# Kernel tuning notes

Measured on AMD Instinct MI355X. Metric: run time of the kernel, lower is better.

## Reference

```python
import jax, jax.numpy as jnp
import numpy as np

D_MODEL = 1024
D_INNER = 4096
K = 127
B, L = 2, 4096

def setup_inputs() -> dict:
    key = jax.random.key(0)
    k1, k2, k3, k4, k5 = jax.random.split(key, 5)
    x = jax.random.normal(k1, (B, L, D_MODEL), dtype=jnp.float32)
    # in_proj: Linear(d, 2*m) -> weight [2m, d] (torch convention)
    w_in = jax.random.normal(k2, (2 * D_INNER, D_MODEL), dtype=jnp.float32) * (1.0 / np.sqrt(D_MODEL))
    # depthwise conv weight: [m, 1, k] in torch; store as [m, k]
    w_dw = jax.random.normal(k3, (D_INNER, K), dtype=jnp.float32) * (1.0 / np.sqrt(K))
    b_dw = jax.random.normal(k4, (D_INNER,), dtype=jnp.float32) * 0.01
    # out_proj: Linear(m, d) -> weight [d, m]
    w_out = jax.random.normal(k5, (D_MODEL, D_INNER), dtype=jnp.float32) * (1.0 / np.sqrt(D_INNER))
    return {"x": x, "w_in": w_in, "w_dw": w_dw, "b_dw": b_dw, "w_out": w_out}

def _causal_dwconv(v, w_dw, b_dw):
    # v: [B, L, m]; causal depthwise conv with kernel K
    # pad K-1 on the left only (equivalent to torch pad=K-1 then [..., :L])
    v_bcl = jnp.transpose(v, (0, 2, 1))  # [B, m, L]
    out = jax.lax.conv_general_dilated(
        v_bcl,
        w_dw[:, None, :],  # [m, 1, K]
        window_strides=(1,),
        padding=[(K - 1, 0)],
        feature_group_count=D_INNER,
        dimension_numbers=("NCH", "OIH", "NCH"),
    )
    out = out + b_dw[None, :, None]
    return jnp.transpose(out, (0, 2, 1))  # [B, L, m]

def reference(x, w_in, w_dw, b_dw, w_out):
    vg = jnp.einsum("bld,ed->ble", x, w_in)  # [B, L, 2m]
    v, g = jnp.split(vg, 2, axis=-1)
    v = _causal_dwconv(v, w_dw, b_dw)
    y = jax.nn.silu(v) * jax.nn.silu(g)
    return jnp.einsum("blm,dm->bld", y, w_out)
```

## Files before the change

### kernel.cpp

```cpp
#include <hip/hip_runtime.h>
#include <hip/hip_bf16.h>
#include <cstdint>
#include <cstddef>

typedef __fp16 f16_t;
typedef __attribute__((ext_vector_type(8))) __fp16 f16x8;
typedef __attribute__((ext_vector_type(4))) __fp16 f16x4;
typedef __attribute__((ext_vector_type(2))) __fp16 h2_t;
typedef __attribute__((ext_vector_type(4))) float floatx4;

__device__ __forceinline__ void async_copy_16B(const void* g, void* l) {
  __builtin_amdgcn_global_load_lds(
      (const __attribute__((address_space(1))) void*)g,
      (__attribute__((address_space(3))) void*)l, 16, 0, 0);
}

__global__ __launch_bounds__(256) void prep(
    const float* __restrict__ x, const float* __restrict__ w_in,
    const float* __restrict__ w_out, const float* __restrict__ w_dw,
    f16_t* __restrict__ x_h, f16_t* __restrict__ wi_h,
    f16_t* __restrict__ wo_h, h2_t* __restrict__ wp) {
  const int tid = blockIdx.x * 256 + threadIdx.x;
  if (tid < 5242880) {
    const float* src;
    f16_t* dst;
    int off;
    if (tid < 2097152) {
      src = x; dst = x_h; off = tid;
    } else if (tid < 4194304) {
      src = w_in; dst = wi_h; off = tid - 2097152;
    } else {
      src = w_out; dst = wo_h; off = tid - 4194304;
    }
    const float4 v = *(const float4*)(src + (size_t)off * 4);
    f16x4 o;
    o.x = (f16_t)v.x; o.y = (f16_t)v.y; o.z = (f16_t)v.z; o.w = (f16_t)v.w;
    *(f16x4*)(dst + (size_t)off * 4) = o;
  } else {
    const int idx = tid - 5242880;
    if (idx < 128 * 4096) {
      const int p = idx >> 12;
      const int c = idx & 4095;
      float a, b;
      if (p < 126) {
        a = w_dw[c * 127 + p]; b = w_dw[c * 127 + p + 1];
      } else if (p == 126) {
        a = w_dw[c * 127 + 126]; b = 0.f;
      } else {
        a = 0.f; b = w_dw[c * 127 + 0];
      }
      h2_t w;
      w.x = (f16_t)a; w.y = (f16_t)b;
      wp[idx] = w;
    }
  }
}

template <int BN_, typename OutT>
__global__ __launch_bounds__(256) void gemm_bt64(
    const f16_t* __restrict__ A, const f16_t* __restrict__ B,
    OutT* __restrict__ C, int M, int N, int K) {
  constexpr int BM_ = 128;
  constexpr int FI = (BN_ == 128) ? 4 : 2;
  constexpr int FJ = 4;
  constexpr int ACH = BM_ * 8;
  constexpr int CH = (BM_ + BN_) * 8;
  constexpr int CPT = CH / 256;

  __shared__ f16_t smem[(BM_ + BN_) * 64];
  f16_t* const As0 = smem;
  f16_t* const As1 = smem + BM_ * 32;
  f16_t* const Bs0 = smem + BM_ * 64;
  f16_t* const Bs1 = smem + BM_ * 64 + BN_ * 32;

  const int t = threadIdx.x;
  const int lane = t & 63;
  const int wave = t >> 6;
  const int m0 = blockIdx.y * BM_;
  const int n0 = blockIdx.x * BN_;
  const int wr = (BN_ == 128) ? (wave >> 1) * 64 : wave * 32;
  const int wc = (BN_ == 128) ? (wave & 1) * 64 : 0;
  const int fr = lane & 15;
  const int fk = (lane >> 4) * 8;

  floatx4 acc[FI][FJ] = {};

  const int kTiles = K / 64;
  for (int kt = 0; kt < kTiles; ++kt) {
    const int k0 = kt * 64;
    __syncthreads();
#pragma unroll
    for (int it = 0; it < CPT; ++it) {
      const int p = it * 256 + t;
      const f16_t* gsrc;
      if (p < BM_ * 4) {
        const int row = p >> 2, kc = (p & 3) * 8;
        gsrc = A + (size_t)(m0 + row) * K + k0 + kc;
      } else if (p < ACH) {
        const int q = p - BM_ * 4;
        const int row = q >> 2, kc = 32 + (q & 3) * 8;
        gsrc = A + (size_t)(m0 + row) * K + k0 + kc;
      } else if (p < ACH + BN_ * 4) {
        const int q = p - ACH;
        const int row = q >> 2, kc = (q & 3) * 8;
        gsrc = B + (size_t)(n0 + row) * K + k0 + kc;
      } else {
        const int q = p - ACH - BN_ * 4;
        const int row = q >> 2, kc = 32 + (q & 3) * 8;
        gsrc = B + (size_t)(n0 + row) * K + k0 + kc;
      }
      async_copy_16B(gsrc, smem + p * 8);
    }
    __syncthreads();

    f16x8 af[FI][2], bfr[FJ][2];
#pragma unroll
    for (int i = 0; i < FI; ++i) {
      const int r = (wr + i * 16 + fr) * 32 + fk;
      af[i][0] = *(const f16x8*)(As0 + r);
      af[i][1] = *(const f16x8*)(As1 + r);
    }
#pragma unroll
    for (int j = 0; j < FJ; ++j) {
      const int r = (wc + j * 16 + fr) * 32 + fk;
      bfr[j][0] = *(const f16x8*)(Bs0 + r);
      bfr[j][1] = *(const f16x8*)(Bs1 + r);
    }
#pragma unroll
    for (int h = 0; h < 2; ++h)
#pragma unroll
      for (int i = 0; i < FI; ++i)
#pragma unroll
        for (int j = 0; j < FJ; ++j)
          acc[i][j] = __builtin_amdgcn_mfma_f32_16x16x32_f16(
              af[i][h], bfr[j][h], acc[i][j], 0, 0, 0);
  }

  const int cr = (lane >> 4) * 4;
  const int cc = lane & 15;
#pragma unroll
  for (int i = 0; i < FI; ++i)
#pragma unroll
    for (int j = 0; j < FJ; ++j)
#pragma unroll
      for (int r = 0; r < 4; ++r) {
        const int row = m0 + wr + i * 16 + cr + r;
        const int col = n0 + wc + j * 16 + cc;
        C[(size_t)row * N + col] = (OutT)acc[i][j][r];
      }
}

#define CONV_L 128
#define CPAIRS 127

__global__ __launch_bounds__(256) void conv_gate(
    const f16_t* __restrict__ vg, const h2_t* __restrict__ wp,
    const float* __restrict__ b_dw, f16_t* __restrict__ y) {
  __shared__ uint32_t vtp[CPAIRS * 64];
  __shared__ uint32_t wpl[128 * 64];
  const int t = threadIdx.x;
  const int lane = t & 63;
  const int wave = t >> 6;
  const int c0 = blockIdx.x * 64;
  const int lt = blockIdx.y & 31;
  const int b = blockIdx.y >> 5;
  const int l0 = lt * CONV_L;

#pragma unroll
  for (int it = 0; it < 8; ++it) {
    const int q = it * 256 + t;
    async_copy_16B(wp + (size_t)(q >> 4) * 4096 + c0 + (q & 15) * 4,
                   wpl + q * 4);
  }
  for (int q = t; q < CPAIRS * 8; q += 256) {
    const int m = q >> 3;
    const int oc = (q & 7) * 8;
    const int le = l0 - 126 + 2 * m;
    uint4 a = make_uint4(0u, 0u, 0u, 0u);
    uint4 bb = make_uint4(0u, 0u, 0u, 0u);
    if (le >= 0) {
      const size_t base = (size_t)(b * 4096 + le) * 8192 + c0 + oc;
      a = *(const uint4*)(vg + base);
      bb = *(const uint4*)(vg + base + 8192);
    }
    uint32_t* dst = vtp + m * 64 + oc;
    const uint32_t aw[4] = {a.x, a.y, a.z, a.w};
    const uint32_t bw[4] = {bb.x, bb.y, bb.z, bb.w};
#pragma unroll
    for (int i = 0; i < 4; ++i) {
      dst[2 * i] = (aw[i] & 0xFFFFu) | (bw[i] << 16);
      dst[2 * i + 1] = (aw[i] >> 16) | (bw[i] & 0xFFFF0000u);
    }
  }
  __syncthreads();

  const int c = c0 + lane;
  const float bias = b_dw[c];
  float acc[32];
#pragma unroll
  for (int i = 0; i < 32; ++i) acc[i] = bias;

  const uint32_t* vbase = vtp + wave * 16 * 64 + lane;
  const uint32_t* wbase = wpl + lane;

  h2_t ring[17];
#pragma unroll
  for (int m = 0; m < 17; ++m)
    ring[m] = __builtin_bit_cast(h2_t, vbase[m * 64]);

  {
    const h2_t w0 = __builtin_bit_cast(h2_t, wbase[127 * 64]);
#pragma unroll
    for (int h = 0; h < 16; ++h)
      acc[2 * h + 1] =
          __builtin_amdgcn_fdot2(w0, ring[h], acc[2 * h + 1], false);
  }

#pragma unroll
  for (int k = 0; k < 64; ++k) {
    const h2_t we = __builtin_bit_cast(h2_t, wbase[(2 * k) * 64]);
#pragma unroll
    for (int h = 0; h < 16; ++h)
      acc[2 * h] =
          __builtin_amdgcn_fdot2(we, ring[(k + h) % 17], acc[2 * h], false);
    if (k < 63) {
      const h2_t wo = __builtin_bit_cast(h2_t, wbase[(2 * k + 1) * 64]);
#pragma unroll
      for (int h = 0; h < 16; ++h)
        acc[2 * h + 1] = __builtin_amdgcn_fdot2(wo, ring[(k + 1 + h) % 17],
                                                acc[2 * h + 1], false);
      if (k < 62)
        ring[k % 17] = __builtin_bit_cast(h2_t, vbase[(17 + k) * 64]);
    }
  }

  const int lb = l0 + wave * 32;
  const f16_t* gp = vg + (size_t)(b * 4096 + lb) * 8192 + 4096 + c;
  f16_t* yp = y + (size_t)(b * 4096 + lb) * 4096 + c;
#pragma unroll
  for (int i = 0; i < 32; ++i) {
    const float gv = (float)gp[(size_t)i * 8192];
    const float v = acc[i];
    const float sv = v / (1.f + __expf(-v));
    const float sg = gv / (1.f + __expf(-gv));
    yp[(size_t)i * 4096] = (f16_t)(sv * sg);
  }
}

extern "C" void kernel_launch(void* const* d_in, const int* in_sizes, int n_in,
                              void* d_out, int out_size, void* d_ws,
                              size_t ws_size, hipStream_t stream) {
  const float* x     = (const float*)d_in[0];
  const float* w_in  = (const float*)d_in[1];
  const float* w_dw  = (const float*)d_in[2];
  const float* b_dw  = (const float*)d_in[3];
  const float* w_out = (const float*)d_in[4];
  float* out = (float*)d_out;

  char* p = (char*)d_ws;
  f16_t* x_h  = (f16_t*)p; p += (size_t)8192 * 1024 * 2;
  f16_t* wi_h = (f16_t*)p; p += (size_t)8192 * 1024 * 2;
  f16_t* wo_h = (f16_t*)p; p += (size_t)1024 * 4096 * 2;
  h2_t*  wp   = (h2_t*)p;  p += (size_t)128 * 4096 * 4;
  f16_t* vg   = (f16_t*)p; p += (size_t)8192 * 8192 * 2;
  f16_t* y    = (f16_t*)p; p += (size_t)8192 * 4096 * 2;

  prep<<<22528, 256, 0, stream>>>(x, w_in, w_out, w_dw, x_h, wi_h, wo_h, wp);

  gemm_bt64<128, f16_t><<<dim3(64, 64), 256, 0, stream>>>(x_h, wi_h, vg,
                                                          8192, 8192, 1024);
  conv_gate<<<dim3(64, 64), 256, 0, stream>>>(vg, wp, b_dw, y);
  gemm_bt64<64, float><<<dim3(16, 64), 256, 0, stream>>>(y, wo_h, out,
                                                         8192, 1024, 4096);
}
```

Before: 506.4 us.

## Add K=128 tiled out-projection GEMM and prefetch gate values before conv

After: 488.0 us. -3.6%, faster.

```diff
diff --git a/kernel.cpp b/kernel.cpp
--- a/kernel.cpp
+++ b/kernel.cpp
@@ -150,6 +150,82 @@
       }
 }
 
+__global__ __launch_bounds__(256) void gemm_bt_k128(
+    const f16_t* __restrict__ A, const f16_t* __restrict__ B,
+    float* __restrict__ C, int M, int N, int K) {
+  constexpr int BM_ = 128, BN_ = 64, KP = 4;
+  constexpr int NA = BM_ * 4 * KP;
+  constexpr int NTOT = (BM_ + BN_) * 4 * KP;
+  constexpr int CPT = NTOT / 256;
+
+  __shared__ f16_t smem[(BM_ + BN_) * 128];
+  const int t = threadIdx.x;
+  const int lane = t & 63;
+  const int wave = t >> 6;
+  const int m0 = blockIdx.y * BM_;
+  const int n0 = blockIdx.x * BN_;
+  const int wr = wave * 32;
+  const int fr = lane & 15;
+  const int fk = (lane >> 4) * 8;
+
+  floatx4 acc[2][4] = {};
+
+  const int kTiles = K / 128;
+  for (int kt = 0; kt < kTiles; ++kt) {
+    const int k0 = kt * 128;
+    __syncthreads();
+#pragma unroll
+    for (int it = 0; it < CPT; ++it) {
+      const int p = it * 256 + t;
+      const f16_t* gsrc;
+      if (p < NA) {
+        const int h = p >> 9;
+        const int r = (p >> 2) & (BM_ - 1);
+        const int kc = h * 32 + (p & 3) * 8;
+        gsrc = A + (size_t)(m0 + r) * K + k0 + kc;
+      } else {
+        const int q = p - NA;
+        const int h = q >> 8;
+        const int r = (q >> 2) & (BN_ - 1);
+        const int kc = h * 32 + (q & 3) * 8;
+        gsrc = B + (size_t)(n0 + r) * K + k0 + kc;
+      }
+      async_copy_16B(gsrc, smem + p * 8);
+    }
+    __syncthreads();
+
+#pragma unroll
+    for (int h = 0; h < KP; ++h) {
+      f16x8 af[2], bf[4];
+#pragma unroll
+      for (int i = 0; i < 2; ++i)
+        af[i] = *(const f16x8*)(smem + h * BM_ * 32 + (wr + i * 16 + fr) * 32 + fk);
+#pragma unroll
+      for (int j = 0; j < 4; ++j)
+        bf[j] = *(const f16x8*)(smem + NA * 8 + h * BN_ * 32 + (j * 16 + fr) * 32 + fk);
+#pragma unroll
+      for (int i = 0; i < 2; ++i)
+#pragma unroll
+        for (int j = 0; j < 4; ++j)
+          acc[i][j] = __builtin_amdgcn_mfma_f32_16x16x32_f16(
+              af[i], bf[j], acc[i][j], 0, 0, 0);
+    }
+  }
+
+  const int cr = (lane >> 4) * 4;
+  const int cc = lane & 15;
+#pragma unroll
+  for (int i = 0; i < 2; ++i)
+#pragma unroll
+    for (int j = 0; j < 4; ++j)
+#pragma unroll
+      for (int r = 0; r < 4; ++r) {
+        const int row = m0 + wr + i * 16 + cr + r;
+        const int col = n0 + j * 16 + cc;
+        C[(size_t)row * N + col] = acc[i][j][r];
+      }
+}
+
 #define CONV_L 128
 #define CPAIRS 127
 
@@ -192,9 +268,16 @@
       dst[2 * i + 1] = (aw[i] >> 16) | (bw[i] & 0xFFFF0000u);
     }
   }
+
+  const int c = c0 + lane;
+  const int lb = l0 + wave * 32;
+  const f16_t* gp = vg + (size_t)(b * 4096 + lb) * 8192 + 4096 + c;
+  f16_t gvals[32];
+#pragma unroll
+  for (int i = 0; i < 32; ++i) gvals[i] = gp[(size_t)i * 8192];
+
   __syncthreads();
 
-  const int c = c0 + lane;
   const float bias = b_dw[c];
   float acc[32];
 #pragma unroll
@@ -234,12 +317,10 @@
     }
   }
 
-  const int lb = l0 + wave * 32;
-  const f16_t* gp = vg + (size_t)(b * 4096 + lb) * 8192 + 4096 + c;
   f16_t* yp = y + (size_t)(b * 4096 + lb) * 4096 + c;
 #pragma unroll
   for (int i = 0; i < 32; ++i) {
-    const float gv = (float)gp[(size_t)i * 8192];
+    const float gv = (float)gvals[i];
     const float v = acc[i];
     const float sv = v / (1.f + __expf(-v));
     const float sg = gv / (1.f + __expf(-gv));
@@ -270,6 +351,6 @@
   gemm_bt64<128, f16_t><<<dim3(64, 64), 256, 0, stream>>>(x_h, wi_h, vg,
                                                           8192, 8192, 1024);
   conv_gate<<<dim3(64, 64), 256, 0, stream>>>(vg, wp, b_dw, y);
-  gemm_bt64<64, float><<<dim3(16, 64), 256, 0, stream>>>(y, wo_h, out,
-                                                         8192, 1024, 4096);
-}
+  gemm_bt_k128<<<dim3(16, 64), 256, 0, stream>>>(y, wo_h, out,
+                                                 8192, 1024, 4096);
+}
```
